# Performance work log

Measured on AMD Instinct MI355X. Metric: run time of the kernel, lower is better.

The kernel has to match this reference:

```python
import jax, jax.numpy as jnp
import numpy as np

TOPK = 13
NUM_CLASSES = 80
ALPHA = 1.0
BETA = 3.0
EPS = 1e-9
K_NEAR = 4
N_BINS = 36  # theta bins: arange(0, 360, 10)


def _dist_max_per_bin(anc_points, gt_pts):
    """gt_pts: (bs,nm,360,2), anc_points: (na,2) -> (bs,nm,na,36) ray targets."""
    d = gt_pts[:, :, None, :, :] - anc_points[None, None, :, None, :]  # (bs,nm,na,360,2)
    dist = jnp.sqrt(jnp.sum(d * d, axis=-1))                           # (bs,nm,na,360)
    ang = jnp.rad2deg(jnp.arctan2(d[..., 1], d[..., 0])) % 360.0       # (bs,nm,na,360)
    theta = jnp.arange(0, 360, 360 // N_BINS).astype(ang.dtype)        # (36,)

    def per_theta(th):
        diff = jnp.abs(ang - th)
        diff = jnp.where(diff > 180.0, 360.0 - diff, diff)
        neg_v, idx = jax.lax.top_k(-diff, K_NEAR)   # 4 nearest-angle contour pts
        val = -neg_v
        dk = jnp.take_along_axis(dist, idx, axis=-1)
        dk = jnp.where(jnp.min(val, axis=-1, keepdims=True) > 3.0, 1e-6, dk)
        return jnp.max(dk, axis=-1)                 # (bs,nm,na)

    dm = jax.lax.map(per_theta, theta)              # (36,bs,nm,na); chunked to bound memory
    return jnp.maximum(jnp.moveaxis(dm, 0, -1), 1e-6)


def _mask_iou(target, pred):
    l_max = jnp.maximum(target, pred)
    l_min = jnp.maximum(jnp.minimum(target, pred), 1e-6)
    return jnp.sum(l_min, -1) / jnp.sum(l_max, -1)


def _forward(pd_scores, pd_bboxes, anc_points, gt_labels, gt_bboxes, mask_gt, gt_coor):
    bs, na, nc = pd_scores.shape
    nm = gt_bboxes.shape[1]
    gl = gt_labels[..., 0]            # (bs,nm) int
    mgt = mask_gt[..., 0]             # (bs,nm) float
    gt_pts = gt_coor.reshape(bs, nm, 360, 2)

    # select_candidates_in_gts: anchor center strictly inside gt box
    lt, rb = gt_bboxes[..., :2], gt_bboxes[..., 2:]
    deltas = jnp.concatenate([anc_points[None, None] - lt[:, :, None],
                              rb[:, :, None] - anc_points[None, None]], axis=-1)
    mask_in_gts = (jnp.min(deltas, -1) > 1e-9).astype(pd_scores.dtype)  # (bs,nm,na)
    mask_sel = (mask_in_gts * mgt[:, :, None]) > 0

    # get_box_metrics_polar (dense over (bs,nm,na) instead of boolean-mask select)
    dist_max = _dist_max_per_bin(anc_points, gt_pts)                    # (bs,nm,na,36)
    overlaps = jnp.where(mask_sel, _mask_iou(dist_max, pd_bboxes[:, None]), 0.0)
    bbox_scores = jnp.take_along_axis(jnp.swapaxes(pd_scores, 1, 2), gl[:, :, None], axis=1)
    bbox_scores = jnp.where(mask_sel, bbox_scores, 0.0)
    align_metric = (bbox_scores ** ALPHA) * (overlaps ** BETA)

    # select_topk_candidates
    _, topk_idxs = jax.lax.top_k(align_metric, TOPK)
    topk_idxs = jnp.where(mgt[:, :, None] > 0, topk_idxs, 0)
    count = jnp.sum(jax.nn.one_hot(topk_idxs, na, dtype=align_metric.dtype), axis=-2)
    mask_topk = jnp.where(count > 1, 0.0, count)
    mask_pos = mask_topk * mask_in_gts * mgt[:, :, None]

    # select_highest_overlaps
    fg = jnp.sum(mask_pos, -2)                                          # (bs,na)
    multi = fg[:, None, :] > 1
    is_max = jnp.moveaxis(jax.nn.one_hot(jnp.argmax(overlaps, 1), nm, dtype=mask_pos.dtype), -1, 1)
    mask_pos = jnp.where(multi, is_max, mask_pos)
    fg_mask = jnp.sum(mask_pos, -2)
    target_gt_idx = jnp.argmax(mask_pos, -2)                            # (bs,na)

    # per-positive ray-distance targets + polar centerness (dense, masked)
    mask_pos_b = mask_pos > 0
    gt_dist = jnp.where(mask_pos_b[..., None], dist_max, 0.0)           # (bs,nm,na,36)
    cent = jnp.sqrt(jnp.min(dist_max, -1) / jnp.max(dist_max, -1))
    centerness_gt = jnp.where(mask_pos_b, cent, 0.0)                    # (bs,nm,na)

    # get_targets
    target_labels = jnp.maximum(jnp.take_along_axis(gl, target_gt_idx, axis=1), 0)
    target_bboxes = jnp.take_along_axis(gt_bboxes, target_gt_idx[..., None], axis=1)
    target_scores = jax.nn.one_hot(target_labels, NUM_CLASSES, dtype=pd_scores.dtype)
    target_scores = jnp.where((fg_mask > 0)[..., None], target_scores, 0.0)

    am = align_metric * mask_pos
    pos_align = jnp.max(am, -1, keepdims=True)
    pos_ov = jnp.max(overlaps * mask_pos, -1, keepdims=True)
    norm_align = jnp.max(am * pos_ov / (pos_align + EPS), -2)[..., None]  # (bs,na,1)
    target_scores = target_scores * norm_align

    return (target_labels, target_bboxes, target_scores, mask_pos_b,
            target_gt_idx, gt_dist, centerness_gt, fg_mask > 0)


def setup_inputs():
    key = jax.random.key(0)
    k = jax.random.split(key, 6)
    bs, nc, nm = 2, 80, 10
    pts, strs = [], []
    for s in (8, 16, 32):  # 640x640 YOLO grid -> 8400 anchors
        n = 640 // s
        yv, xv = np.meshgrid(np.arange(n), np.arange(n), indexing='ij')
        pts.append(np.stack([(xv + 0.5) * s, (yv + 0.5) * s], -1).reshape(-1, 2))
        strs.append(np.full((pts[-1].shape[0], 1), s, dtype=np.float32))
    anc_points = jnp.asarray(np.concatenate(pts).astype(np.float32))
    stride_tensor = jnp.asarray(np.concatenate(strs))
    na = anc_points.shape[0]
    pd_scores = jax.random.uniform(k[0], (bs, na, nc), dtype=jnp.float32)
    pd_bboxes = jax.random.uniform(k[1], (bs, na, 36), dtype=jnp.float32) * 100.0 + 1.0
    gt_labels = jax.random.randint(k[2], (bs, nm, 1), 0, nc)
    ctr = jax.random.uniform(k[3], (bs, nm, 2), dtype=jnp.float32) * 440.0 + 100.0
    wh = jax.random.uniform(k[4], (bs, nm, 2), dtype=jnp.float32) * 140.0 + 40.0
    gt_bboxes = jnp.concatenate([ctr - wh / 2.0, ctr + wh / 2.0], -1)
    th = jnp.arange(360.0) * (jnp.pi / 180.0)
    rad = (jnp.min(wh, -1, keepdims=True) / 2.0) * (0.6 + 0.4 * jax.random.uniform(k[5], (bs, nm, 360), dtype=jnp.float32))
    ray = jnp.stack([jnp.cos(th), jnp.sin(th)], -1)  # (360,2)
    gt_coor = (ctr[:, :, None, :] + rad[..., None] * ray[None, None]).reshape(bs, nm, 720)
    mask_gt = jnp.ones((bs, nm, 1), dtype=jnp.float32).at[1, 7:].set(0.0)
    return dict(pd_scores=pd_scores, pd_bboxes=pd_bboxes, anc_points=anc_points,
                gt_labels=gt_labels, gt_bboxes=gt_bboxes, mask_gt=mask_gt,
                gt_coor=gt_coor, stride_tensor=stride_tensor, ss=640,
                gt_center=ctr, imgsz=640)


def reference(pd_scores, pd_bboxes, anc_points, gt_labels, gt_bboxes, mask_gt, gt_coor, stride_tensor, ss, gt_center, imgsz):
    # ss, gt_center, imgsz, stride_tensor are accepted (as in the torch signature) but unused
    return _forward(pd_scores, pd_bboxes, anc_points, gt_labels, gt_bboxes, mask_gt, gt_coor)
```

## Files before the change

kernel.cpp:

```cpp
#include <hip/hip_runtime.h>

#define BS 2
#define NM 10
#define NA 8400
#define NC 80
#define NBIN 36
#define KTOP 13
#define NPAIR_MAX (BS*NM*NA)

__global__ void k_zero(float4* __restrict__ out4, int n4,
                       float* __restrict__ wf, int nz){
  int i = blockIdx.x*256 + threadIdx.x;
  if (i < n4) out4[i] = make_float4(0.f,0.f,0.f,0.f);
  if (i < nz) wf[i] = 0.f;
}

__global__ void k_masklist(const float* __restrict__ anc, const float* __restrict__ gtb,
                           const float* __restrict__ mgt, int* __restrict__ counter,
                           int* __restrict__ pairs){
  int t = blockIdx.x*256 + threadIdx.x;
  if (t >= BS*NM*NA) return;
  int a = t % NA; int bm = t / NA;
  if (mgt[bm] <= 0.f) return;
  float ax = anc[2*a], ay = anc[2*a+1];
  float lx = gtb[bm*4+0], ly = gtb[bm*4+1];
  float rx = gtb[bm*4+2], ry = gtb[bm*4+3];
  float mind = fminf(fminf(ax-lx, ay-ly), fminf(rx-ax, ry-ay));
  if (mind > 1e-9f){
    int i = atomicAdd(counter, 1);
    pairs[i] = t;
  }
}

__global__ __launch_bounds__(256)
void k_dist(const float* __restrict__ anc, const float* __restrict__ coor,
            const float* __restrict__ pdb, const float* __restrict__ pds,
            const int* __restrict__ gl,
            const int* __restrict__ counter, const int* __restrict__ pairs,
            float* __restrict__ w_align, float* __restrict__ w_ovl,
            float* __restrict__ o_gtdist){
  __shared__ float2 s_da[360];
  __shared__ float  s_m[NBIN*33];
  int tid = threadIdx.x;
  int lane = tid & 63, wave = tid >> 6;
  int cnt = counter[0];
  for (int p = blockIdx.x; p < cnt; p += gridDim.x){
    int t = pairs[p];
    int a = t % NA; int bm = t / NA; int b = bm / NM;
    float ax = anc[2*a], ay = anc[2*a+1];
    const float* cc = coor + bm*720;
    for (int i = tid; i < 360; i += 256){
      float dx = cc[2*i]   - ax;
      float dy = cc[2*i+1] - ay;
      float dist = sqrtf(dx*dx + dy*dy);
      float an = atan2f(dy, dx) * 57.29577951308232f;
      if (an < 0.f) an += 360.f;
      s_da[i] = make_float2(dist, an);
    }
    __syncthreads();
    if (lane < NBIN){
      float th = (float)(lane*10);
      float v0=1e30f, v1=1e30f, v2=1e30f, v3=1e30f;
      float d0=0.f, d1=0.f, d2=0.f, d3=0.f;
      int base = wave*90;
      for (int k = 0; k < 90; k++){
        float2 da = s_da[base + k];
        float diff = fabsf(da.y - th);
        diff = fminf(diff, 360.f - diff);
        if (diff < v3){
          v3 = diff; d3 = da.x;
          if (v3 < v2){ float tv=v2; v2=v3; v3=tv; float td=d2; d2=d3; d3=td; }
          if (v2 < v1){ float tv=v1; v1=v2; v2=tv; float td=d1; d1=d2; d2=td; }
          if (v1 < v0){ float tv=v0; v0=v1; v1=tv; float td=d0; d0=d1; d1=td; }
        }
      }
      int mb = lane*33 + wave*8;
      s_m[mb+0]=v0; s_m[mb+1]=v1; s_m[mb+2]=v2; s_m[mb+3]=v3;
      s_m[mb+4]=d0; s_m[mb+5]=d1; s_m[mb+6]=d2; s_m[mb+7]=d3;
    }
    __syncthreads();
    if (wave == 0){
      float sum_min = 0.f, sum_max = 0.f;
      if (lane < NBIN){
        int mb = lane*33;
        float h0=s_m[mb+0], h1=s_m[mb+8], h2=s_m[mb+16], h3=s_m[mb+24];
        int p0=0, p1=0, p2=0, p3=0;
        float v0m = 0.f, dmax = 0.f;
#pragma unroll
        for (int step = 0; step < 4; step++){
          float bv = h0; int bw = 0;
          if (h1 < bv){ bv = h1; bw = 1; }
          if (h2 < bv){ bv = h2; bw = 2; }
          if (h3 < bv){ bv = h3; bw = 3; }
          float dd;
          if (bw == 0){ dd = s_m[mb+4+p0]; p0++; h0 = (p0<4)? s_m[mb+p0]    : 1e30f; }
          else if (bw == 1){ dd = s_m[mb+12+p1]; p1++; h1 = (p1<4)? s_m[mb+8+p1]  : 1e30f; }
          else if (bw == 2){ dd = s_m[mb+20+p2]; p2++; h2 = (p2<4)? s_m[mb+16+p2] : 1e30f; }
          else             { dd = s_m[mb+28+p3]; p3++; h3 = (p3<4)? s_m[mb+24+p3] : 1e30f; }
          if (step == 0) v0m = bv;
          dmax = fmaxf(dmax, dd);
        }
        float dm = (v0m > 3.0f) ? 1e-6f : dmax;
        float dfin = fmaxf(dm, 1e-6f);
        o_gtdist[(size_t)t*NBIN + lane] = dfin;
        float pr = pdb[((size_t)b*NA + a)*NBIN + lane];
        sum_max = fmaxf(dfin, pr);
        sum_min = fmaxf(fminf(dfin, pr), 1e-6f);
      }
      for (int off = 32; off > 0; off >>= 1){
        sum_min += __shfl_down(sum_min, off);
        sum_max += __shfl_down(sum_max, off);
      }
      if (lane == 0){
        float ov = sum_min / sum_max;
        int cls = gl[bm];
        float sc = pds[((size_t)b*NA + a)*NC + cls];
        w_align[t] = sc * ov * ov * ov;
        w_ovl[t]   = ov;
      }
    }
    __syncthreads();
  }
}

__global__ __launch_bounds__(512)
void k_topk(const float* __restrict__ w_align, float* __restrict__ w_mask){
  int bm = blockIdx.x;
  const float* al = w_align + (size_t)bm*NA;
  int tid = threadIdx.x;
  __shared__ float sv[512*KTOP];
  __shared__ int   si[512*KTOP];
  __shared__ float wv8[8];
  __shared__ int   wi8[8];

  float v[KTOP]; int ix[KTOP];
#pragma unroll
  for (int j = 0; j < KTOP; j++){ v[j] = -1.f; ix[j] = 0x7fffffff; }
  for (int a = tid; a < NA; a += 512){
    float x = al[a];
    if (x > v[KTOP-1]){
      v[KTOP-1] = x; ix[KTOP-1] = a;
#pragma unroll
      for (int j = KTOP-1; j > 0; j--){
        if (v[j] > v[j-1]){
          float tv = v[j-1]; v[j-1] = v[j]; v[j] = tv;
          int   ti = ix[j-1]; ix[j-1] = ix[j]; ix[j] = ti;
        }
      }
    }
  }
#pragma unroll
  for (int j = 0; j < KTOP; j++){ sv[tid*KTOP+j] = v[j]; si[tid*KTOP+j] = ix[j]; }

  int head = 0;
  int lane = tid & 63, wave = tid >> 6;
  for (int r = 0; r < KTOP; r++){
    float cv = sv[tid*KTOP + head];
    int   ci = si[tid*KTOP + head];
    float rv = cv; int ri = ci;
    for (int off = 32; off > 0; off >>= 1){
      float ov = __shfl_down(rv, off);
      int   oi = __shfl_down(ri, off);
      if (ov > rv || (ov == rv && oi < ri)){ rv = ov; ri = oi; }
    }
    if (lane == 0){ wv8[wave] = rv; wi8[wave] = ri; }
    __syncthreads();
    float Wv = wv8[0]; int Wi = wi8[0];
#pragma unroll
    for (int w = 1; w < 8; w++){
      float ov = wv8[w]; int oi = wi8[w];
      if (ov > Wv || (ov == Wv && oi < Wi)){ Wv = ov; Wi = oi; }
    }
    if (ci == Wi && head < KTOP-1) head++;
    if (tid == 0 && Wv > 0.f) w_mask[(size_t)bm*NA + Wi] = 1.f;
    __syncthreads();
  }
}

__global__ void k_final(const float* __restrict__ w_align, const float* __restrict__ w_ovl,
                        float* __restrict__ w_mask,
                        const int* __restrict__ gl, const float* __restrict__ gtb,
                        float* __restrict__ o_labels, float* __restrict__ o_bboxes,
                        float* __restrict__ o_maskpos, float* __restrict__ o_gtidx,
                        float* __restrict__ o_fg,
                        float* __restrict__ w_pa, float* __restrict__ w_po){
  int t = blockIdx.x*256 + threadIdx.x;
  if (t >= BS*NA) return;
  int a = t % NA, b = t / NA;
  float mp[NM];
  int fg = 0;
#pragma unroll
  for (int m = 0; m < NM; m++){
    mp[m] = w_mask[((size_t)(b*NM+m))*NA + a];
    fg += (mp[m] > 0.f) ? 1 : 0;
  }
  if (fg > 1){
    float bv = -1.f; int bi = 0;
#pragma unroll
    for (int m = 0; m < NM; m++){
      float v = w_ovl[((size_t)(b*NM+m))*NA + a];
      if (v > bv){ bv = v; bi = m; }
    }
#pragma unroll
    for (int m = 0; m < NM; m++){
      mp[m] = (m == bi) ? 1.f : 0.f;
      w_mask[((size_t)(b*NM+m))*NA + a] = mp[m];
    }
    fg = 1;
  }
  int tgt = 0;
#pragma unroll
  for (int m = NM-1; m >= 0; m--) if (mp[m] > 0.f) tgt = m;
#pragma unroll
  for (int m = 0; m < NM; m++) o_maskpos[((size_t)(b*NM+m))*NA + a] = mp[m];
  o_gtidx[t] = (float)tgt;
  o_fg[t] = (fg > 0) ? 1.f : 0.f;
  int lbl = gl[b*NM + tgt]; if (lbl < 0) lbl = 0;
  o_labels[t] = (float)lbl;
  const float* bx = gtb + (b*NM + tgt)*4;
  ((float4*)o_bboxes)[t] = make_float4(bx[0], bx[1], bx[2], bx[3]);
  if (fg > 0){
    int bmx = b*NM + tgt;
    float av = w_align[(size_t)bmx*NA + a];
    float ovv = w_ovl[(size_t)bmx*NA + a];
    atomicMax((unsigned int*)&w_pa[bmx], __float_as_uint(av));
    atomicMax((unsigned int*)&w_po[bmx], __float_as_uint(ovv));
  }
}

#define NB_FIX 1024
__global__ void k_fuse(const int* __restrict__ counter, const int* __restrict__ pairs,
                       const float* __restrict__ w_mask, float* __restrict__ o_gtdist,
                       float* __restrict__ o_cent,
                       const float* __restrict__ w_align,
                       const float* __restrict__ w_pa, const float* __restrict__ w_po,
                       const float* __restrict__ o_labels, const float* __restrict__ o_fg,
                       const float* __restrict__ o_gtidx, float* __restrict__ o_scores){
  if (blockIdx.x < NB_FIX){
    int lane = threadIdx.x & 63, wave = threadIdx.x >> 6;
    int cnt = counter[0];
    for (int p = blockIdx.x*4 + wave; p < cnt; p += NB_FIX*4){
      int t = pairs[p];
      float m = w_mask[t];
      float* row = o_gtdist + (size_t)t*NBIN;
      if (m > 0.f){
        float vmin = 1e30f, vmax = 0.f;
        if (lane < NBIN){
          float v = row[lane];
          vmin = v; vmax = v;
        }
        for (int off = 32; off > 0; off >>= 1){
          vmin = fminf(vmin, __shfl_down(vmin, off));
          vmax = fmaxf(vmax, __shfl_down(vmax, off));
        }
        if (lane == 0) o_cent[t] = sqrtf(vmin / vmax);
      } else {
        if (lane < NBIN) row[lane] = 0.f;
      }
    }
  } else {
    int t = (blockIdx.x - NB_FIX)*256 + threadIdx.x;
    if (t < BS*NA && o_fg[t] > 0.f){
      int a = t % NA, b = t / NA;
      int m = (int)o_gtidx[t];
      int bm = b*NM + m;
      float av = w_align[(size_t)bm*NA + a];
      float norm = av * w_po[bm] / (w_pa[bm] + 1e-9f);
      int lbl = (int)o_labels[t];
      o_scores[(size_t)t*NC + lbl] = norm;
    }
  }
}

extern "C" void kernel_launch(void* const* d_in, const int* in_sizes, int n_in,
                              void* d_out, int out_size, void* d_ws, size_t ws_size,
                              hipStream_t stream){
  const float* pds  = (const float*)d_in[0];
  const float* pdb  = (const float*)d_in[1];
  const float* anc  = (const float*)d_in[2];
  const int*   gl   = (const int*)  d_in[3];
  const float* gtb  = (const float*)d_in[4];
  const float* mgt  = (const float*)d_in[5];
  const float* coor = (const float*)d_in[6];

  float* out = (float*)d_out;
  float* o_labels  = out;
  float* o_bboxes  = o_labels + BS*NA;
  float* o_scores  = o_bboxes + BS*NA*4;
  float* o_maskpos = o_scores + (size_t)BS*NA*NC;
  float* o_gtidx   = o_maskpos + BS*NM*NA;
  float* o_gtdist  = o_gtidx + BS*NA;
  float* o_cent    = o_gtdist + (size_t)BS*NM*NA*NBIN;
  float* o_fg      = o_cent + BS*NM*NA;

  float* wf      = (float*)d_ws;
  int*   counter = (int*)d_ws;
  float* w_align = wf + 16;
  float* w_ovl   = w_align + BS*NM*NA;
  float* w_mask  = w_ovl + BS*NM*NA;
  float* w_pa    = w_mask + BS*NM*NA;
  float* w_po    = w_pa + BS*NM;
  int*   w_pairs = (int*)(w_po + BS*NM);

  int n4 = out_size / 4;
  int nz = 16 + 3*BS*NM*NA + 2*BS*NM;
  int nmax = (n4 > nz) ? n4 : nz;
  k_zero<<<(nmax+255)/256, 256, 0, stream>>>((float4*)out, n4, wf, nz);
  k_masklist<<<(BS*NM*NA+255)/256, 256, 0, stream>>>(anc, gtb, mgt, counter, w_pairs);
  k_dist<<<4096, 256, 0, stream>>>(anc, coor, pdb, pds, gl, counter, w_pairs,
                                   w_align, w_ovl, o_gtdist);
  k_topk<<<BS*NM, 512, 0, stream>>>(w_align, w_mask);
  k_final<<<(BS*NA+255)/256, 256, 0, stream>>>(w_align, w_ovl, w_mask, gl, gtb,
                                               o_labels, o_bboxes, o_maskpos, o_gtidx, o_fg,
                                               w_pa, w_po);
  k_fuse<<<NB_FIX + (BS*NA+255)/256, 256, 0, stream>>>(counter, w_pairs, w_mask,
                                                       o_gtdist, o_cent,
                                                       w_align, w_pa, w_po,
                                                       o_labels, o_fg, o_gtidx, o_scores);
}
```

Before: 182.2 us.

## Fuse all stages into one cooperative persistent kernel with grid syncs

Replaces the six separate launches (zero, masklist, dist, topk, final, fuse) with a single cooperative kernel. The stages are separated by grid.sync and use grid-stride loops, with a fixed grid sized from the occupancy query and capped at 1024 blocks. Only the counter is cleared by a small memset before launch. This removes per-launch gaps and tail effects between stages. In exchange the dist stage runs with fewer blocks, top-k uses 256 threads instead of 512, and most blocks sit idle during the top-k phase while waiting at the grid barriers.

```diff
diff --git a/kernel.cpp b/kernel.cpp
--- a/kernel.cpp
+++ b/kernel.cpp
@@ -1,4 +1,7 @@
 #include <hip/hip_runtime.h>
+#include <hip/hip_cooperative_groups.h>
+
+namespace cg = cooperative_groups;
 
 #define BS 2
 #define NM 10
@@ -6,241 +9,247 @@
 #define NC 80
 #define NBIN 36
 #define KTOP 13
-#define NPAIR_MAX (BS*NM*NA)
-
-__global__ void k_zero(float4* __restrict__ out4, int n4,
-                       float* __restrict__ wf, int nz){
-  int i = blockIdx.x*256 + threadIdx.x;
-  if (i < n4) out4[i] = make_float4(0.f,0.f,0.f,0.f);
-  if (i < nz) wf[i] = 0.f;
-}
-
-__global__ void k_masklist(const float* __restrict__ anc, const float* __restrict__ gtb,
-                           const float* __restrict__ mgt, int* __restrict__ counter,
-                           int* __restrict__ pairs){
-  int t = blockIdx.x*256 + threadIdx.x;
-  if (t >= BS*NM*NA) return;
-  int a = t % NA; int bm = t / NA;
-  if (mgt[bm] <= 0.f) return;
-  float ax = anc[2*a], ay = anc[2*a+1];
-  float lx = gtb[bm*4+0], ly = gtb[bm*4+1];
-  float rx = gtb[bm*4+2], ry = gtb[bm*4+3];
-  float mind = fminf(fminf(ax-lx, ay-ly), fminf(rx-ax, ry-ay));
-  if (mind > 1e-9f){
-    int i = atomicAdd(counter, 1);
-    pairs[i] = t;
-  }
-}
-
-__global__ __launch_bounds__(256)
-void k_dist(const float* __restrict__ anc, const float* __restrict__ coor,
-            const float* __restrict__ pdb, const float* __restrict__ pds,
-            const int* __restrict__ gl,
-            const int* __restrict__ counter, const int* __restrict__ pairs,
-            float* __restrict__ w_align, float* __restrict__ w_ovl,
-            float* __restrict__ o_gtdist){
-  __shared__ float2 s_da[360];
-  __shared__ float  s_m[NBIN*33];
-  int tid = threadIdx.x;
+
+__global__ __launch_bounds__(256, 4)
+void k_mega(const float* __restrict__ pds, const float* __restrict__ pdb,
+            const float* __restrict__ anc, const int* __restrict__ gl,
+            const float* __restrict__ gtb, const float* __restrict__ mgt,
+            const float* __restrict__ coor,
+            float* __restrict__ out, float* __restrict__ wf){
+  cg::grid_group grid = cg::this_grid();
+
+  float* o_labels  = out;
+  float* o_bboxes  = out + 16800;
+  float* o_scores  = out + 84000;
+  float* o_maskpos = out + 1428000;
+  float* o_gtidx   = out + 1596000;
+  float* o_gtdist  = out + 1612800;
+  float* o_cent    = out + 7660800;
+  float* o_fg      = out + 7828800;
+
+  int*   counter = (int*)wf;
+  float* w_align = wf + 16;
+  float* w_ovl   = w_align + BS*NM*NA;
+  float* w_mask  = w_ovl + BS*NM*NA;
+  float* w_pa    = w_mask + BS*NM*NA;
+  float* w_po    = w_pa + BS*NM;
+  int*   w_pairs = (int*)(w_po + BS*NM);
+
+  __shared__ __align__(16) float spool[6672];
+
+  int tid  = threadIdx.x;
   int lane = tid & 63, wave = tid >> 6;
-  int cnt = counter[0];
-  for (int p = blockIdx.x; p < cnt; p += gridDim.x){
-    int t = pairs[p];
-    int a = t % NA; int bm = t / NA; int b = bm / NM;
-    float ax = anc[2*a], ay = anc[2*a+1];
-    const float* cc = coor + bm*720;
-    for (int i = tid; i < 360; i += 256){
-      float dx = cc[2*i]   - ax;
-      float dy = cc[2*i+1] - ay;
-      float dist = sqrtf(dx*dx + dy*dy);
-      float an = atan2f(dy, dx) * 57.29577951308232f;
-      if (an < 0.f) an += 360.f;
-      s_da[i] = make_float2(dist, an);
-    }
-    __syncthreads();
-    if (lane < NBIN){
-      float th = (float)(lane*10);
-      float v0=1e30f, v1=1e30f, v2=1e30f, v3=1e30f;
-      float d0=0.f, d1=0.f, d2=0.f, d3=0.f;
-      int base = wave*90;
-      for (int k = 0; k < 90; k++){
-        float2 da = s_da[base + k];
-        float diff = fabsf(da.y - th);
-        diff = fminf(diff, 360.f - diff);
-        if (diff < v3){
-          v3 = diff; d3 = da.x;
-          if (v3 < v2){ float tv=v2; v2=v3; v3=tv; float td=d2; d2=d3; d3=td; }
-          if (v2 < v1){ float tv=v1; v1=v2; v2=tv; float td=d1; d1=d2; d2=td; }
-          if (v1 < v0){ float tv=v0; v0=v1; v1=tv; float td=d0; d0=d1; d1=td; }
-        }
-      }
-      int mb = lane*33 + wave*8;
-      s_m[mb+0]=v0; s_m[mb+1]=v1; s_m[mb+2]=v2; s_m[mb+3]=v3;
-      s_m[mb+4]=d0; s_m[mb+5]=d1; s_m[mb+6]=d2; s_m[mb+7]=d3;
-    }
-    __syncthreads();
-    if (wave == 0){
-      float sum_min = 0.f, sum_max = 0.f;
+  int gsz  = gridDim.x * 256;
+  int gtid = blockIdx.x * 256 + tid;
+
+  {
+    float4* out4 = (float4*)out;
+    const int n4 = (16800+67200+1344000+168000+16800+6048000+168000+16800)/4;
+    for (int i = gtid; i < n4; i += gsz) out4[i] = make_float4(0.f,0.f,0.f,0.f);
+    float4* w4 = (float4*)(wf + 16);
+    const int nw4 = (3*BS*NM*NA + 2*BS*NM)/4;
+    for (int i = gtid; i < nw4; i += gsz) w4[i] = make_float4(0.f,0.f,0.f,0.f);
+    for (int t = gtid; t < BS*NM*NA; t += gsz){
+      int a = t % NA; int bm = t / NA;
+      if (mgt[bm] <= 0.f) continue;
+      float ax = anc[2*a], ay = anc[2*a+1];
+      float lx = gtb[bm*4+0], ly = gtb[bm*4+1];
+      float rx = gtb[bm*4+2], ry = gtb[bm*4+3];
+      float mind = fminf(fminf(ax-lx, ay-ly), fminf(rx-ax, ry-ay));
+      if (mind > 1e-9f){
+        int i = atomicAdd(counter, 1);
+        w_pairs[i] = t;
+      }
+    }
+  }
+  grid.sync();
+
+  {
+    float2* s_da = (float2*)spool;
+    float*  s_m  = spool + 720;
+    int cnt = counter[0];
+    for (int p = blockIdx.x; p < cnt; p += gridDim.x){
+      int t = w_pairs[p];
+      int a = t % NA; int bm = t / NA; int b = bm / NM;
+      float ax = anc[2*a], ay = anc[2*a+1];
+      const float* cc = coor + bm*720;
+      for (int i = tid; i < 360; i += 256){
+        float dx = cc[2*i]   - ax;
+        float dy = cc[2*i+1] - ay;
+        float dist = sqrtf(dx*dx + dy*dy);
+        float an = atan2f(dy, dx) * 57.29577951308232f;
+        if (an < 0.f) an += 360.f;
+        s_da[i] = make_float2(dist, an);
+      }
+      __syncthreads();
       if (lane < NBIN){
-        int mb = lane*33;
-        float h0=s_m[mb+0], h1=s_m[mb+8], h2=s_m[mb+16], h3=s_m[mb+24];
-        int p0=0, p1=0, p2=0, p3=0;
-        float v0m = 0.f, dmax = 0.f;
-#pragma unroll
-        for (int step = 0; step < 4; step++){
-          float bv = h0; int bw = 0;
-          if (h1 < bv){ bv = h1; bw = 1; }
-          if (h2 < bv){ bv = h2; bw = 2; }
-          if (h3 < bv){ bv = h3; bw = 3; }
-          float dd;
-          if (bw == 0){ dd = s_m[mb+4+p0]; p0++; h0 = (p0<4)? s_m[mb+p0]    : 1e30f; }
-          else if (bw == 1){ dd = s_m[mb+12+p1]; p1++; h1 = (p1<4)? s_m[mb+8+p1]  : 1e30f; }
-          else if (bw == 2){ dd = s_m[mb+20+p2]; p2++; h2 = (p2<4)? s_m[mb+16+p2] : 1e30f; }
-          else             { dd = s_m[mb+28+p3]; p3++; h3 = (p3<4)? s_m[mb+24+p3] : 1e30f; }
-          if (step == 0) v0m = bv;
-          dmax = fmaxf(dmax, dd);
-        }
-        float dm = (v0m > 3.0f) ? 1e-6f : dmax;
-        float dfin = fmaxf(dm, 1e-6f);
-        o_gtdist[(size_t)t*NBIN + lane] = dfin;
-        float pr = pdb[((size_t)b*NA + a)*NBIN + lane];
-        sum_max = fmaxf(dfin, pr);
-        sum_min = fmaxf(fminf(dfin, pr), 1e-6f);
-      }
+        float th = (float)(lane*10);
+        float v0=1e30f, v1=1e30f, v2=1e30f, v3=1e30f;
+        float d0=0.f, d1=0.f, d2=0.f, d3=0.f;
+        int base = wave*90;
+        for (int k = 0; k < 90; k++){
+          float2 da = s_da[base + k];
+          float diff = fabsf(da.y - th);
+          diff = fminf(diff, 360.f - diff);
+          if (diff < v3){
+            v3 = diff; d3 = da.x;
+            if (v3 < v2){ float tv=v2; v2=v3; v3=tv; float td=d2; d2=d3; d3=td; }
+            if (v2 < v1){ float tv=v1; v1=v2; v2=tv; float td=d1; d1=d2; d2=td; }
+            if (v1 < v0){ float tv=v0; v0=v1; v1=tv; float td=d0; d0=d1; d1=td; }
+          }
+        }
+        int mb = lane*33 + wave*8;
+        s_m[mb+0]=v0; s_m[mb+1]=v1; s_m[mb+2]=v2; s_m[mb+3]=v3;
+        s_m[mb+4]=d0; s_m[mb+5]=d1; s_m[mb+6]=d2; s_m[mb+7]=d3;
+      }
+      __syncthreads();
+      if (wave == 0){
+        float sum_min = 0.f, sum_max = 0.f;
+        if (lane < NBIN){
+          int mb = lane*33;
+          float h0=s_m[mb+0], h1=s_m[mb+8], h2=s_m[mb+16], h3=s_m[mb+24];
+          int p0=0, p1=0, p2=0, p3=0;
+          float v0m = 0.f, dmax = 0.f;
+#pragma unroll
+          for (int step = 0; step < 4; step++){
+            float bv = h0; int bw = 0;
+            if (h1 < bv){ bv = h1; bw = 1; }
+            if (h2 < bv){ bv = h2; bw = 2; }
+            if (h3 < bv){ bv = h3; bw = 3; }
+            float dd;
+            if (bw == 0){ dd = s_m[mb+4+p0]; p0++; h0 = (p0<4)? s_m[mb+p0]    : 1e30f; }
+            else if (bw == 1){ dd = s_m[mb+12+p1]; p1++; h1 = (p1<4)? s_m[mb+8+p1]  : 1e30f; }
+            else if (bw == 2){ dd = s_m[mb+20+p2]; p2++; h2 = (p2<4)? s_m[mb+16+p2] : 1e30f; }
+            else             { dd = s_m[mb+28+p3]; p3++; h3 = (p3<4)? s_m[mb+24+p3] : 1e30f; }
+            if (step == 0) v0m = bv;
+            dmax = fmaxf(dmax, dd);
+          }
+          float dm = (v0m > 3.0f) ? 1e-6f : dmax;
+          float dfin = fmaxf(dm, 1e-6f);
+          o_gtdist[(size_t)t*NBIN + lane] = dfin;
+          float pr = pdb[((size_t)b*NA + a)*NBIN + lane];
+          sum_max = fmaxf(dfin, pr);
+          sum_min = fmaxf(fminf(dfin, pr), 1e-6f);
+        }
+        for (int off = 32; off > 0; off >>= 1){
+          sum_min += __shfl_down(sum_min, off);
+          sum_max += __shfl_down(sum_max, off);
+        }
+        if (lane == 0){
+          float ov = sum_min / sum_max;
+          int cls = gl[bm];
+          float sc = pds[((size_t)b*NA + a)*NC + cls];
+          w_align[t] = sc * ov * ov * ov;
+          w_ovl[t]   = ov;
+        }
+      }
+      __syncthreads();
+    }
+  }
+  grid.sync();
+
+  if (blockIdx.x < BS*NM){
+    int bm = blockIdx.x;
+    const float* al = w_align + (size_t)bm*NA;
+    float* sv = spool;
+    int*   si = (int*)(spool + 3328);
+    float* wv4 = spool + 6656;
+    int*   wi4 = (int*)(spool + 6660);
+
+    float v[KTOP]; int ix[KTOP];
+#pragma unroll
+    for (int j = 0; j < KTOP; j++){ v[j] = -1.f; ix[j] = 0x7fffffff; }
+    for (int a = tid; a < NA; a += 256){
+      float x = al[a];
+      if (x > v[KTOP-1]){
+        v[KTOP-1] = x; ix[KTOP-1] = a;
+#pragma unroll
+        for (int j = KTOP-1; j > 0; j--){
+          if (v[j] > v[j-1]){
+            float tv = v[j-1]; v[j-1] = v[j]; v[j] = tv;
+            int   ti = ix[j-1]; ix[j-1] = ix[j]; ix[j] = ti;
+          }
+        }
+      }
+    }
+#pragma unroll
+    for (int j = 0; j < KTOP; j++){ sv[tid*KTOP+j] = v[j]; si[tid*KTOP+j] = ix[j]; }
+
+    int head = 0;
+    for (int r = 0; r < KTOP; r++){
+      float cv = sv[tid*KTOP + head];
+      int   ci = si[tid*KTOP + head];
+      float rv = cv; int ri = ci;
       for (int off = 32; off > 0; off >>= 1){
-        sum_min += __shfl_down(sum_min, off);
-        sum_max += __shfl_down(sum_max, off);
-      }
-      if (lane == 0){
-        float ov = sum_min / sum_max;
-        int cls = gl[bm];
-        float sc = pds[((size_t)b*NA + a)*NC + cls];
-        w_align[t] = sc * ov * ov * ov;
-        w_ovl[t]   = ov;
-      }
-    }
-    __syncthreads();
-  }
-}
-
-__global__ __launch_bounds__(512)
-void k_topk(const float* __restrict__ w_align, float* __restrict__ w_mask){
-  int bm = blockIdx.x;
-  const float* al = w_align + (size_t)bm*NA;
-  int tid = threadIdx.x;
-  __shared__ float sv[512*KTOP];
-  __shared__ int   si[512*KTOP];
-  __shared__ float wv8[8];
-  __shared__ int   wi8[8];
-
-  float v[KTOP]; int ix[KTOP];
-#pragma unroll
-  for (int j = 0; j < KTOP; j++){ v[j] = -1.f; ix[j] = 0x7fffffff; }
-  for (int a = tid; a < NA; a += 512){
-    float x = al[a];
-    if (x > v[KTOP-1]){
-      v[KTOP-1] = x; ix[KTOP-1] = a;
-#pragma unroll
-      for (int j = KTOP-1; j > 0; j--){
-        if (v[j] > v[j-1]){
-          float tv = v[j-1]; v[j-1] = v[j]; v[j] = tv;
-          int   ti = ix[j-1]; ix[j-1] = ix[j]; ix[j] = ti;
-        }
-      }
-    }
-  }
-#pragma unroll
-  for (int j = 0; j < KTOP; j++){ sv[tid*KTOP+j] = v[j]; si[tid*KTOP+j] = ix[j]; }
-
-  int head = 0;
-  int lane = tid & 63, wave = tid >> 6;
-  for (int r = 0; r < KTOP; r++){
-    float cv = sv[tid*KTOP + head];
-    int   ci = si[tid*KTOP + head];
-    float rv = cv; int ri = ci;
-    for (int off = 32; off > 0; off >>= 1){
-      float ov = __shfl_down(rv, off);
-      int   oi = __shfl_down(ri, off);
-      if (ov > rv || (ov == rv && oi < ri)){ rv = ov; ri = oi; }
-    }
-    if (lane == 0){ wv8[wave] = rv; wi8[wave] = ri; }
-    __syncthreads();
-    float Wv = wv8[0]; int Wi = wi8[0];
-#pragma unroll
-    for (int w = 1; w < 8; w++){
-      float ov = wv8[w]; int oi = wi8[w];
-      if (ov > Wv || (ov == Wv && oi < Wi)){ Wv = ov; Wi = oi; }
-    }
-    if (ci == Wi && head < KTOP-1) head++;
-    if (tid == 0 && Wv > 0.f) w_mask[(size_t)bm*NA + Wi] = 1.f;
-    __syncthreads();
-  }
-}
-
-__global__ void k_final(const float* __restrict__ w_align, const float* __restrict__ w_ovl,
-                        float* __restrict__ w_mask,
-                        const int* __restrict__ gl, const float* __restrict__ gtb,
-                        float* __restrict__ o_labels, float* __restrict__ o_bboxes,
-                        float* __restrict__ o_maskpos, float* __restrict__ o_gtidx,
-                        float* __restrict__ o_fg,
-                        float* __restrict__ w_pa, float* __restrict__ w_po){
-  int t = blockIdx.x*256 + threadIdx.x;
-  if (t >= BS*NA) return;
-  int a = t % NA, b = t / NA;
-  float mp[NM];
-  int fg = 0;
-#pragma unroll
-  for (int m = 0; m < NM; m++){
-    mp[m] = w_mask[((size_t)(b*NM+m))*NA + a];
-    fg += (mp[m] > 0.f) ? 1 : 0;
-  }
-  if (fg > 1){
-    float bv = -1.f; int bi = 0;
+        float ov = __shfl_down(rv, off);
+        int   oi = __shfl_down(ri, off);
+        if (ov > rv || (ov == rv && oi < ri)){ rv = ov; ri = oi; }
+      }
+      if (lane == 0){ wv4[wave] = rv; wi4[wave] = ri; }
+      __syncthreads();
+      float Wv = wv4[0]; int Wi = wi4[0];
+#pragma unroll
+      for (int w = 1; w < 4; w++){
+        float ov = wv4[w]; int oi = wi4[w];
+        if (ov > Wv || (ov == Wv && oi < Wi)){ Wv = ov; Wi = oi; }
+      }
+      if (ci == Wi && head < KTOP-1) head++;
+      if (tid == 0 && Wv > 0.f) w_mask[(size_t)bm*NA + Wi] = 1.f;
+      __syncthreads();
+    }
+  }
+  grid.sync();
+
+  for (int t = gtid; t < BS*NA; t += gsz){
+    int a = t % NA, b = t / NA;
+    float mp[NM];
+    int fg = 0;
 #pragma unroll
     for (int m = 0; m < NM; m++){
-      float v = w_ovl[((size_t)(b*NM+m))*NA + a];
-      if (v > bv){ bv = v; bi = m; }
-    }
-#pragma unroll
-    for (int m = 0; m < NM; m++){
-      mp[m] = (m == bi) ? 1.f : 0.f;
-      w_mask[((size_t)(b*NM+m))*NA + a] = mp[m];
-    }
-    fg = 1;
-  }
-  int tgt = 0;
-#pragma unroll
-  for (int m = NM-1; m >= 0; m--) if (mp[m] > 0.f) tgt = m;
-#pragma unroll
-  for (int m = 0; m < NM; m++) o_maskpos[((size_t)(b*NM+m))*NA + a] = mp[m];
-  o_gtidx[t] = (float)tgt;
-  o_fg[t] = (fg > 0) ? 1.f : 0.f;
-  int lbl = gl[b*NM + tgt]; if (lbl < 0) lbl = 0;
-  o_labels[t] = (float)lbl;
-  const float* bx = gtb + (b*NM + tgt)*4;
-  ((float4*)o_bboxes)[t] = make_float4(bx[0], bx[1], bx[2], bx[3]);
-  if (fg > 0){
-    int bmx = b*NM + tgt;
-    float av = w_align[(size_t)bmx*NA + a];
-    float ovv = w_ovl[(size_t)bmx*NA + a];
-    atomicMax((unsigned int*)&w_pa[bmx], __float_as_uint(av));
-    atomicMax((unsigned int*)&w_po[bmx], __float_as_uint(ovv));
-  }
-}
-
-#define NB_FIX 1024
-__global__ void k_fuse(const int* __restrict__ counter, const int* __restrict__ pairs,
-                       const float* __restrict__ w_mask, float* __restrict__ o_gtdist,
-                       float* __restrict__ o_cent,
-                       const float* __restrict__ w_align,
-                       const float* __restrict__ w_pa, const float* __restrict__ w_po,
-                       const float* __restrict__ o_labels, const float* __restrict__ o_fg,
-                       const float* __restrict__ o_gtidx, float* __restrict__ o_scores){
-  if (blockIdx.x < NB_FIX){
-    int lane = threadIdx.x & 63, wave = threadIdx.x >> 6;
+      mp[m] = w_mask[((size_t)(b*NM+m))*NA + a];
+      fg += (mp[m] > 0.f) ? 1 : 0;
+    }
+    if (fg > 1){
+      float bv = -1.f; int bi = 0;
+#pragma unroll
+      for (int m = 0; m < NM; m++){
+        float v = w_ovl[((size_t)(b*NM+m))*NA + a];
+        if (v > bv){ bv = v; bi = m; }
+      }
+#pragma unroll
+      for (int m = 0; m < NM; m++){
+        mp[m] = (m == bi) ? 1.f : 0.f;
+        w_mask[((size_t)(b*NM+m))*NA + a] = mp[m];
+      }
+      fg = 1;
+    }
+    int tgt = 0;
+#pragma unroll
+    for (int m = NM-1; m >= 0; m--) if (mp[m] > 0.f) tgt = m;
+#pragma unroll
+    for (int m = 0; m < NM; m++) o_maskpos[((size_t)(b*NM+m))*NA + a] = mp[m];
+    o_gtidx[t] = (float)tgt;
+    o_fg[t] = (fg > 0) ? 1.f : 0.f;
+    int lbl = gl[b*NM + tgt]; if (lbl < 0) lbl = 0;
+    o_labels[t] = (float)lbl;
+    const float* bx = gtb + (b*NM + tgt)*4;
+    ((float4*)o_bboxes)[t] = make_float4(bx[0], bx[1], bx[2], bx[3]);
+    if (fg > 0){
+      int bmx = b*NM + tgt;
+      float av  = w_align[(size_t)bmx*NA + a];
+      float ovv = w_ovl[(size_t)bmx*NA + a];
+      atomicMax((unsigned int*)&w_pa[bmx], __float_as_uint(av));
+      atomicMax((unsigned int*)&w_po[bmx], __float_as_uint(ovv));
+    }
+  }
+  grid.sync();
+
+  {
     int cnt = counter[0];
-    for (int p = blockIdx.x*4 + wave; p < cnt; p += NB_FIX*4){
-      int t = pairs[p];
+    int wid = blockIdx.x*4 + wave;
+    int nw  = gridDim.x*4;
+    for (int p = wid; p < cnt; p += nw){
+      int t = w_pairs[p];
       float m = w_mask[t];
       float* row = o_gtdist + (size_t)t*NBIN;
       if (m > 0.f){
@@ -258,16 +267,16 @@
         if (lane < NBIN) row[lane] = 0.f;
       }
     }
-  } else {
-    int t = (blockIdx.x - NB_FIX)*256 + threadIdx.x;
-    if (t < BS*NA && o_fg[t] > 0.f){
-      int a = t % NA, b = t / NA;
-      int m = (int)o_gtidx[t];
-      int bm = b*NM + m;
-      float av = w_align[(size_t)bm*NA + a];
-      float norm = av * w_po[bm] / (w_pa[bm] + 1e-9f);
-      int lbl = (int)o_labels[t];
-      o_scores[(size_t)t*NC + lbl] = norm;
+    for (int t = gtid; t < BS*NA; t += gsz){
+      if (o_fg[t] > 0.f){
+        int a = t % NA, b = t / NA;
+        int m = (int)o_gtidx[t];
+        int bm = b*NM + m;
+        float av = w_align[(size_t)bm*NA + a];
+        float norm = av * w_po[bm] / (w_pa[bm] + 1e-9f);
+        int lbl = (int)o_labels[t];
+        o_scores[(size_t)t*NC + lbl] = norm;
+      }
     }
   }
 }
@@ -284,37 +293,20 @@
   const float* coor = (const float*)d_in[6];
 
   float* out = (float*)d_out;
-  float* o_labels  = out;
-  float* o_bboxes  = o_labels + BS*NA;
-  float* o_scores  = o_bboxes + BS*NA*4;
-  float* o_maskpos = o_scores + (size_t)BS*NA*NC;
-  float* o_gtidx   = o_maskpos + BS*NM*NA;
-  float* o_gtdist  = o_gtidx + BS*NA;
-  float* o_cent    = o_gtdist + (size_t)BS*NM*NA*NBIN;
-  float* o_fg      = o_cent + BS*NM*NA;
-
-  float* wf      = (float*)d_ws;
-  int*   counter = (int*)d_ws;
-  float* w_align = wf + 16;
-  float* w_ovl   = w_align + BS*NM*NA;
-  float* w_mask  = w_ovl + BS*NM*NA;
-  float* w_pa    = w_mask + BS*NM*NA;
-  float* w_po    = w_pa + BS*NM;
-  int*   w_pairs = (int*)(w_po + BS*NM);
-
-  int n4 = out_size / 4;
-  int nz = 16 + 3*BS*NM*NA + 2*BS*NM;
-  int nmax = (n4 > nz) ? n4 : nz;
-  k_zero<<<(nmax+255)/256, 256, 0, stream>>>((float4*)out, n4, wf, nz);
-  k_masklist<<<(BS*NM*NA+255)/256, 256, 0, stream>>>(anc, gtb, mgt, counter, w_pairs);
-  k_dist<<<4096, 256, 0, stream>>>(anc, coor, pdb, pds, gl, counter, w_pairs,
-                                   w_align, w_ovl, o_gtdist);
-  k_topk<<<BS*NM, 512, 0, stream>>>(w_align, w_mask);
-  k_final<<<(BS*NA+255)/256, 256, 0, stream>>>(w_align, w_ovl, w_mask, gl, gtb,
-                                               o_labels, o_bboxes, o_maskpos, o_gtidx, o_fg,
-                                               w_pa, w_po);
-  k_fuse<<<NB_FIX + (BS*NA+255)/256, 256, 0, stream>>>(counter, w_pairs, w_mask,
-                                                       o_gtdist, o_cent,
-                                                       w_align, w_pa, w_po,
-                                                       o_labels, o_fg, o_gtidx, o_scores);
+  float* wf  = (float*)d_ws;
+
+  hipMemsetAsync(wf, 0, 4, stream);
+
+  int nb = 0;
+  hipOccupancyMaxActiveBlocksPerMultiprocessor(&nb, (const void*)k_mega, 256, 0);
+  if (nb < 1) nb = 1;
+  int grid = nb * 256;
+  if (grid > 1024) grid = 1024;
+  if (grid < 256)  grid = 256;
+
+  void* args[] = { (void*)&pds, (void*)&pdb, (void*)&anc, (void*)&gl,
+                   (void*)&gtb, (void*)&mgt, (void*)&coor,
+                   (void*)&out, (void*)&wf };
+  hipLaunchCooperativeKernel((const void*)k_mega, dim3(grid), dim3(256),
+                             args, 0, stream);
 }
```

Measured after the change: 624.2 us. +242.6%, slower.

## Replace atomic pair list with analytic anchor-rectangle enumeration and fuse zeroing

Applied to the files above, without the earlier changes.

Removes the zero and mask-list kernels. Each block now works out, per (gt, stride level), the rectangle of anchor grid cells inside the box and maps a flat pair index to an anchor through a prefix sum, so there is no atomic compaction and no pair array. Zeroing moves into k_dist as a grid-stride prologue that only writes non-candidate gtdist rows and the needed outputs, which cuts redundant full-output clears. It relies on anchors forming a regular 8/16/32-stride grid over 640, and it changes pair order. It also halves the k_fuse fixed-block count.

```diff
diff --git a/kernel.cpp b/kernel.cpp
--- a/kernel.cpp
+++ b/kernel.cpp
@@ -6,46 +6,119 @@
 #define NC 80
 #define NBIN 36
 #define KTOP 13
-#define NPAIR_MAX (BS*NM*NA)
-
-__global__ void k_zero(float4* __restrict__ out4, int n4,
-                       float* __restrict__ wf, int nz){
-  int i = blockIdx.x*256 + threadIdx.x;
-  if (i < n4) out4[i] = make_float4(0.f,0.f,0.f,0.f);
-  if (i < nz) wf[i] = 0.f;
-}
-
-__global__ void k_masklist(const float* __restrict__ anc, const float* __restrict__ gtb,
-                           const float* __restrict__ mgt, int* __restrict__ counter,
-                           int* __restrict__ pairs){
-  int t = blockIdx.x*256 + threadIdx.x;
-  if (t >= BS*NM*NA) return;
-  int a = t % NA; int bm = t / NA;
-  if (mgt[bm] <= 0.f) return;
-  float ax = anc[2*a], ay = anc[2*a+1];
-  float lx = gtb[bm*4+0], ly = gtb[bm*4+1];
-  float rx = gtb[bm*4+2], ry = gtb[bm*4+3];
-  float mind = fminf(fminf(ax-lx, ay-ly), fminf(rx-ax, ry-ay));
-  if (mind > 1e-9f){
-    int i = atomicAdd(counter, 1);
-    pairs[i] = t;
-  }
+#define NRECT (BS*NM*3)
+
+__device__ __forceinline__ void rect_setup(int tid,
+    const float* __restrict__ gtb, const float* __restrict__ mgt,
+    int* sx0, int* sy0, int* scx, int* scum, int* sn, int* sbase){
+  if (tid < NRECT){
+    int bm = tid/3, lv = tid - bm*3;
+    int cnt = 0, x0 = 0, y0 = 0, cx = 0, n = 0, base = 0;
+    if (mgt[bm] > 0.f){
+      float s = (float)(8 << lv);
+      n = 640 >> (3 + lv);
+      base = (lv == 0) ? 0 : ((lv == 1) ? 6400 : 8000);
+      float lx = gtb[bm*4+0], ly = gtb[bm*4+1];
+      float rx = gtb[bm*4+2], ry = gtb[bm*4+3];
+      int a0 = (int)ceilf(lx/s - 0.5f); a0 = min(max(a0, 0), n);
+      while (a0 > 0   &&  (((a0-1)+0.5f)*s - lx > 1e-9f)) a0--;
+      while (a0 < n   && !(((a0  )+0.5f)*s - lx > 1e-9f)) a0++;
+      int a1 = (int)floorf(rx/s - 0.5f); a1 = min(max(a1, -1), n-1);
+      while (a1 < n-1 &&  (rx - ((a1+1)+0.5f)*s > 1e-9f)) a1++;
+      while (a1 >= 0  && !(rx - ((a1  )+0.5f)*s > 1e-9f)) a1--;
+      int b0 = (int)ceilf(ly/s - 0.5f); b0 = min(max(b0, 0), n);
+      while (b0 > 0   &&  (((b0-1)+0.5f)*s - ly > 1e-9f)) b0--;
+      while (b0 < n   && !(((b0  )+0.5f)*s - ly > 1e-9f)) b0++;
+      int b1 = (int)floorf(ry/s - 0.5f); b1 = min(max(b1, -1), n-1);
+      while (b1 < n-1 &&  (ry - ((b1+1)+0.5f)*s > 1e-9f)) b1++;
+      while (b1 >= 0  && !(ry - ((b1  )+0.5f)*s > 1e-9f)) b1--;
+      cx = max(0, a1 - a0 + 1);
+      int cy = max(0, b1 - b0 + 1);
+      cnt = cx * cy;
+      x0 = a0; y0 = b0;
+    }
+    sx0[tid] = x0; sy0[tid] = y0; scx[tid] = cx;
+    scum[tid] = cnt; sn[tid] = n; sbase[tid] = base;
+  }
+  __syncthreads();
+  if (tid == 0){
+    int acc = 0;
+    for (int r = 0; r < NRECT; r++){ int c = scum[r]; scum[r] = acc; acc += c; }
+    scum[NRECT] = acc;
+  }
+  __syncthreads();
+}
+
+__device__ __forceinline__ int pair_from_p(int p,
+    const int* sx0, const int* sy0, const int* scx,
+    const int* scum, const int* sn, const int* sbase){
+  int r = 0;
+  while (r < NRECT-1 && scum[r+1] <= p) r++;
+  int idx = p - scum[r];
+  int cx = scx[r];
+  int yi = idx / cx;
+  int xi = idx - yi*cx;
+  int a = sbase[r] + (sy0[r] + yi)*sn[r] + (sx0[r] + xi);
+  int bm = r/3;
+  return bm*NA + a;
 }
 
 __global__ __launch_bounds__(256)
-void k_dist(const float* __restrict__ anc, const float* __restrict__ coor,
-            const float* __restrict__ pdb, const float* __restrict__ pds,
-            const int* __restrict__ gl,
-            const int* __restrict__ counter, const int* __restrict__ pairs,
-            float* __restrict__ w_align, float* __restrict__ w_ovl,
-            float* __restrict__ o_gtdist){
+void k_dist(const float* __restrict__ pds, const float* __restrict__ pdb,
+            const float* __restrict__ anc, const int* __restrict__ gl,
+            const float* __restrict__ gtb, const float* __restrict__ mgt,
+            const float* __restrict__ coor,
+            float* __restrict__ out, float* __restrict__ wf){
+  float* o_scores  = out + 84000;
+  float* o_gtdist  = out + 1612800;
+  float* o_cent    = out + 7660800;
+  float* w_align = wf + 16;
+  float* w_ovl   = w_align + BS*NM*NA;
+  float* w_mask  = w_ovl + BS*NM*NA;
+  float* w_pa    = w_mask + BS*NM*NA;
+
+  __shared__ int sx0[NRECT], sy0[NRECT], scx[NRECT], scum[NRECT+1], sn[NRECT], sbase[NRECT];
   __shared__ float2 s_da[360];
   __shared__ float  s_m[NBIN*33];
+
   int tid = threadIdx.x;
   int lane = tid & 63, wave = tid >> 6;
-  int cnt = counter[0];
-  for (int p = blockIdx.x; p < cnt; p += gridDim.x){
-    int t = pairs[p];
+  int gsz  = gridDim.x * 256;
+  int gtid = blockIdx.x * 256 + tid;
+
+  rect_setup(tid, gtb, mgt, sx0, sy0, scx, scum, sn, sbase);
+  int total = scum[NRECT];
+
+  {
+    float4 z = make_float4(0.f, 0.f, 0.f, 0.f);
+    float4* sc4 = (float4*)o_scores;
+    for (int i = gtid; i < (BS*NA*NC)/4; i += gsz) sc4[i] = z;
+    float4* ce4 = (float4*)o_cent;
+    for (int i = gtid; i < (BS*NM*NA)/4; i += gsz) ce4[i] = z;
+    if (gtid < 2*BS*NM) w_pa[gtid] = 0.f;
+    for (int t = gtid; t < BS*NM*NA; t += gsz){
+      int a = t % NA; int bm = t / NA;
+      w_mask[t] = 0.f;
+      bool inpair = false;
+      if (mgt[bm] > 0.f){
+        float ax = anc[2*a], ay = anc[2*a+1];
+        float lx = gtb[bm*4+0], ly = gtb[bm*4+1];
+        float rx = gtb[bm*4+2], ry = gtb[bm*4+3];
+        float mind = fminf(fminf(ax-lx, ay-ly), fminf(rx-ax, ry-ay));
+        inpair = (mind > 1e-9f);
+      }
+      if (!inpair){
+        w_align[t] = 0.f;
+        w_ovl[t]   = 0.f;
+        float4* row = (float4*)(o_gtdist + (size_t)t*NBIN);
+#pragma unroll
+        for (int j = 0; j < 9; j++) row[j] = z;
+      }
+    }
+  }
+
+  for (int p = blockIdx.x; p < total; p += gridDim.x){
+    int t = pair_from_p(p, sx0, sy0, scx, scum, sn, sbase);
     int a = t % NA; int bm = t / NA; int b = bm / NM;
     float ax = anc[2*a], ay = anc[2*a+1];
     const float* cc = coor + bm*720;
@@ -221,15 +294,15 @@
   ((float4*)o_bboxes)[t] = make_float4(bx[0], bx[1], bx[2], bx[3]);
   if (fg > 0){
     int bmx = b*NM + tgt;
-    float av = w_align[(size_t)bmx*NA + a];
+    float av  = w_align[(size_t)bmx*NA + a];
     float ovv = w_ovl[(size_t)bmx*NA + a];
     atomicMax((unsigned int*)&w_pa[bmx], __float_as_uint(av));
     atomicMax((unsigned int*)&w_po[bmx], __float_as_uint(ovv));
   }
 }
 
-#define NB_FIX 1024
-__global__ void k_fuse(const int* __restrict__ counter, const int* __restrict__ pairs,
+#define NB_FIX 512
+__global__ void k_fuse(const float* __restrict__ gtb, const float* __restrict__ mgt,
                        const float* __restrict__ w_mask, float* __restrict__ o_gtdist,
                        float* __restrict__ o_cent,
                        const float* __restrict__ w_align,
@@ -237,10 +310,13 @@
                        const float* __restrict__ o_labels, const float* __restrict__ o_fg,
                        const float* __restrict__ o_gtidx, float* __restrict__ o_scores){
   if (blockIdx.x < NB_FIX){
-    int lane = threadIdx.x & 63, wave = threadIdx.x >> 6;
-    int cnt = counter[0];
-    for (int p = blockIdx.x*4 + wave; p < cnt; p += NB_FIX*4){
-      int t = pairs[p];
+    __shared__ int sx0[NRECT], sy0[NRECT], scx[NRECT], scum[NRECT+1], sn[NRECT], sbase[NRECT];
+    int tid = threadIdx.x;
+    rect_setup(tid, gtb, mgt, sx0, sy0, scx, scum, sn, sbase);
+    int total = scum[NRECT];
+    int lane = tid & 63, wave = tid >> 6;
+    for (int p = blockIdx.x*4 + wave; p < total; p += NB_FIX*4){
+      int t = pair_from_p(p, sx0, sy0, scx, scum, sn, sbase);
       float m = w_mask[t];
       float* row = o_gtdist + (size_t)t*NBIN;
       if (m > 0.f){
@@ -294,26 +370,18 @@
   float* o_fg      = o_cent + BS*NM*NA;
 
   float* wf      = (float*)d_ws;
-  int*   counter = (int*)d_ws;
   float* w_align = wf + 16;
   float* w_ovl   = w_align + BS*NM*NA;
   float* w_mask  = w_ovl + BS*NM*NA;
   float* w_pa    = w_mask + BS*NM*NA;
   float* w_po    = w_pa + BS*NM;
-  int*   w_pairs = (int*)(w_po + BS*NM);
-
-  int n4 = out_size / 4;
-  int nz = 16 + 3*BS*NM*NA + 2*BS*NM;
-  int nmax = (n4 > nz) ? n4 : nz;
-  k_zero<<<(nmax+255)/256, 256, 0, stream>>>((float4*)out, n4, wf, nz);
-  k_masklist<<<(BS*NM*NA+255)/256, 256, 0, stream>>>(anc, gtb, mgt, counter, w_pairs);
-  k_dist<<<4096, 256, 0, stream>>>(anc, coor, pdb, pds, gl, counter, w_pairs,
-                                   w_align, w_ovl, o_gtdist);
+
+  k_dist<<<4096, 256, 0, stream>>>(pds, pdb, anc, gl, gtb, mgt, coor, out, wf);
   k_topk<<<BS*NM, 512, 0, stream>>>(w_align, w_mask);
   k_final<<<(BS*NA+255)/256, 256, 0, stream>>>(w_align, w_ovl, w_mask, gl, gtb,
                                                o_labels, o_bboxes, o_maskpos, o_gtidx, o_fg,
                                                w_pa, w_po);
-  k_fuse<<<NB_FIX + (BS*NA+255)/256, 256, 0, stream>>>(counter, w_pairs, w_mask,
+  k_fuse<<<NB_FIX + (BS*NA+255)/256, 256, 0, stream>>>(gtb, mgt, w_mask,
                                                        o_gtdist, o_cent,
                                                        w_align, w_pa, w_po,
                                                        o_labels, o_fg, o_gtidx, o_scores);
```

Result: slower. 191.0 us (+4.8%).
